# Kernel optimization log

Measured on AMD Instinct MI355X. Metric: run time of the kernel, lower is better.

The kernel has to match this reference:

```python
import jax, jax.numpy as jnp
import numpy as np

EPS = 1e-5
B, NA, T, D, H, L, DFF, E = 4, 64, 128, 128, 8, 3, 512, 65536
NN = T * NA  # nodes per graph = t*n after reshape(b, t*n, f)
DH = D // H


def _layer_norm(x, g, b):
    m = x.mean(-1, keepdims=True)
    v = ((x - m) ** 2).mean(-1, keepdims=True)
    return (x - m) * jax.lax.rsqrt(v + EPS) * g + b


def _pos_encoding(t, d):
    pos = jnp.arange(t, dtype=jnp.float32)[:, None]
    i = jnp.arange(0, d, 2, dtype=jnp.float32)
    ang = pos * jnp.exp(-jnp.log(10000.0) * i / d)
    pe = jnp.zeros((t, d), jnp.float32)
    return pe.at[:, 0::2].set(jnp.sin(ang)).at[:, 1::2].set(jnp.cos(ang))


def _forward(all_hist_feat, edge_weight, hist_w, hist_b,
             attn_wq, attn_bq, attn_wk, attn_bk, attn_wv, attn_bv, attn_wo, attn_bo,
             ln1_g, ln1_b, ff_w1, ff_b1, ff_w2, ff_b2, ln2_g, ln2_b,
             bn_g, bn_b, lin_graph_w, lin_graph_b, edge_index):
    b, n, t, _ = all_hist_feat.shape
    # history embedding: Linear(3, D)  -> [b, n, t, D]
    x = all_hist_feat @ hist_w + hist_b
    # sinusoidal positional encoding over the time axis
    out_e = x + _pos_encoding(t, D)
    scale = 1.0 / jnp.sqrt(jnp.asarray(DH, jnp.float32))
    for l in range(L):  # small fixed layer count
        q = out_e @ attn_wq[l] + attn_bq[l]
        k = out_e @ attn_wk[l] + attn_bk[l]
        v = out_e @ attn_wv[l] + attn_bv[l]
        qh = q.reshape(b, n, t, H, DH)
        kh = k.reshape(b, n, t, H, DH)
        vh = v.reshape(b, n, t, H, DH)
        scores = jnp.einsum('bnqhd,bnkhd->bnhqk', qh, kh) * scale
        attn = jax.nn.softmax(scores, axis=-1)
        o = jnp.einsum('bnhqk,bnkhd->bnqhd', attn, vh).reshape(b, n, t, D)
        o = o @ attn_wo[l] + attn_bo[l]
        h1 = _layer_norm(out_e + o, ln1_g[l], ln1_b[l])
        ff = jax.nn.relu(h1 @ ff_w1[l] + ff_b1[l]) @ ff_w2[l] + ff_b2[l]
        out_e = _layer_norm(h1 + ff, ln2_g[l], ln2_b[l])
    # graph stage: nodes are (time, agent) pairs, index = time*n + agent
    graph_w = out_e.transpose(0, 2, 1, 3).reshape(b, t * n, D)
    graph_x = x.transpose(0, 2, 1, 3).reshape(b, t * n, D)
    # GCNConv_Fixed_W (no self loops, no normalize): per-node score then
    # edge-weighted scatter-add from source to target (PyG convention)
    s = (graph_w * graph_x).sum(-1)  # [b, t*n]
    src, dst = edge_index[:, 0], edge_index[:, 1]

    def agg(s_b, src_b, dst_b, ew_b):
        return jax.ops.segment_sum(ew_b * s_b[src_b], dst_b, num_segments=NN)

    graph_out = jax.vmap(agg)(s, src, dst, edge_weight)  # [b, t*n]
    g = graph_out.reshape(b, t, n)
    # BatchNorm2d(1) on [b, 1, n, t]: single channel -> global batch stats
    m = g.mean()
    var = g.var()
    g = (g - m) * jax.lax.rsqrt(var + EPS) * bn_g[0] + bn_b[0]
    g4 = g.transpose(0, 2, 1)[..., None]  # [b, n, t, 1]
    return g4 @ lin_graph_w + lin_graph_b  # [b, n, t, D]


def setup_inputs() -> dict:
    keys = iter(jax.random.split(jax.random.key(0), 64))

    def nrm(shape, scale):
        return jax.random.normal(next(keys), shape, jnp.float32) * scale

    inp = {
        'all_hist_feat': nrm((B, NA, T, 3), 1.0),
        'edge_index': jax.random.randint(next(keys), (B, 2, E), 0, NN, jnp.int32),
        'edge_weight': jax.random.uniform(next(keys), (B, E), jnp.float32),
        'hist_w': nrm((3, D), 0.5), 'hist_b': nrm((D,), 0.02),
        'attn_wq': nrm((L, D, D), D ** -0.5), 'attn_bq': jnp.zeros((L, D)),
        'attn_wk': nrm((L, D, D), D ** -0.5), 'attn_bk': jnp.zeros((L, D)),
        'attn_wv': nrm((L, D, D), D ** -0.5), 'attn_bv': jnp.zeros((L, D)),
        'attn_wo': nrm((L, D, D), D ** -0.5), 'attn_bo': jnp.zeros((L, D)),
        'ln1_g': jnp.ones((L, D)), 'ln1_b': jnp.zeros((L, D)),
        'ff_w1': nrm((L, D, DFF), D ** -0.5), 'ff_b1': jnp.zeros((L, DFF)),
        'ff_w2': nrm((L, DFF, D), DFF ** -0.5), 'ff_b2': jnp.zeros((L, D)),
        'ln2_g': jnp.ones((L, D)), 'ln2_b': jnp.zeros((L, D)),
        'bn_g': jnp.ones((1,)), 'bn_b': jnp.zeros((1,)),
        'lin_graph_w': nrm((1, D), 1.0), 'lin_graph_b': jnp.zeros((D,)),
    }
    return inp


def reference(all_hist_feat, edge_index, edge_weight, hist_w, hist_b,
              attn_wq, attn_bq, attn_wk, attn_bk, attn_wv, attn_bv, attn_wo, attn_bo,
              ln1_g, ln1_b, ff_w1, ff_b1, ff_w2, ff_b2, ln2_g, ln2_b,
              bn_g, bn_b, lin_graph_w, lin_graph_b):
    return _forward(all_hist_feat, edge_weight, hist_w, hist_b,
                    attn_wq, attn_bq, attn_wk, attn_bk, attn_wv, attn_bv, attn_wo, attn_bo,
                    ln1_g, ln1_b, ff_w1, ff_b1, ff_w2, ff_b2, ln2_g, ln2_b,
                    bn_g, bn_b, lin_graph_w, lin_graph_b, edge_index)
```

## Files before the change

kernel.cpp:

```cpp
#include <hip/hip_runtime.h>
#include <hip/hip_bf16.h>
#include <math.h>

#define EPS_ 1e-5f
constexpr int B_ = 4, NA = 64, T_ = 128, D_ = 128, H_ = 8, L_ = 3, DFF = 512, E_ = 65536;
constexpr int DH = D_ / H_;
constexpr int NN = T_ * NA;
constexpr int NTOT = B_ * NA * T_;
constexpr int QLD = 384;
constexpr size_t NE_ = (size_t)NTOT * D_;

typedef __bf16 bf16x8 __attribute__((ext_vector_type(8)));
typedef float f32x4 __attribute__((ext_vector_type(4)));

__global__ __launch_bounds__(256) void embed_kernel(
    const float* __restrict__ hist, const float* __restrict__ w,
    const float* __restrict__ b, float* __restrict__ x, float* __restrict__ e) {
  int idx = blockIdx.x * 256 + threadIdx.x;
  if (idx >= NTOT * D_) return;
  int d = idx & (D_ - 1);
  int r = idx >> 7;
  int t = r & (T_ - 1);
  const float* hp = hist + (size_t)r * 3;
  float acc = b[d];
  acc += hp[0] * w[0 * D_ + d];
  acc += hp[1] * w[1 * D_ + d];
  acc += hp[2] * w[2 * D_ + d];
  x[idx] = acc;
  int p = d >> 1;
  float ang = (float)t * expf(-logf(10000.f) * (2.f * (float)p) / (float)D_);
  float pe = (d & 1) ? cosf(ang) : sinf(ang);
  e[idx] = acc + pe;
}

__global__ __launch_bounds__(256) void convert_weights(
    const float* __restrict__ wq, const float* __restrict__ wk,
    const float* __restrict__ wv, const float* __restrict__ wo,
    const float* __restrict__ w1, const float* __restrict__ w2,
    __bf16* __restrict__ hi, __bf16* __restrict__ lo) {
  const int LW = 196608;
  int idx = blockIdx.x * 256 + threadIdx.x;
  if (idx >= L_ * LW) return;
  int l = idx / LW;
  int rem = idx - l * LW;
  float src;
  int n, k, K, segoff;
  if (rem < 49152) {
    n = rem >> 7; k = rem & 127; K = 128; segoff = 0;
    int which = n >> 7, nl = n & 127;
    const float* W = (which == 0) ? wq : (which == 1) ? wk : wv;
    src = W[(size_t)l * 16384 + k * 128 + nl];
  } else if (rem < 65536) {
    int r2 = rem - 49152;
    n = r2 >> 7; k = r2 & 127; K = 128; segoff = 49152;
    src = wo[(size_t)l * 16384 + k * 128 + n];
  } else if (rem < 131072) {
    int r2 = rem - 65536;
    n = r2 >> 7; k = r2 & 127; K = 128; segoff = 65536;
    src = w1[(size_t)l * 65536 + k * 512 + n];
  } else {
    int r2 = rem - 131072;
    n = r2 >> 9; k = r2 & 511; K = 512; segoff = 131072;
    src = w2[(size_t)l * 65536 + k * 128 + n];
  }
  int nt = n >> 4, kt = k >> 5;
  int lane = ((k >> 3) & 3) * 16 + (n & 15);
  int j = k & 7;
  int dst = l * LW + segoff + ((nt * (K / 32) + kt) * 64 + lane) * 8 + j;
  __bf16 h = (__bf16)src;
  hi[dst] = h;
  lo[dst] = (__bf16)(src - (float)h);
}

__global__ __launch_bounds__(256) void bias_pack(
    const float* __restrict__ bq, const float* __restrict__ bk,
    const float* __restrict__ bv, float* __restrict__ pb) {
  int idx = blockIdx.x * 256 + threadIdx.x;
  if (idx >= L_ * QLD) return;
  int l = idx / QLD, n = idx - l * QLD;
  int which = n >> 7, nl = n & 127;
  const float* src = (which == 0) ? bq : (which == 1) ? bk : bv;
  pb[idx] = src[l * 128 + nl];
}

__device__ __forceinline__ void split8(const float* __restrict__ p,
                                       bf16x8& hi, bf16x8& lo) {
  float4 x0 = *(const float4*)p;
  float4 x1 = *(const float4*)(p + 4);
  float xv[8] = {x0.x, x0.y, x0.z, x0.w, x1.x, x1.y, x1.z, x1.w};
#pragma unroll
  for (int j = 0; j < 8; ++j) {
    __bf16 h = (__bf16)xv[j];
    hi[j] = h;
    lo[j] = (__bf16)(xv[j] - (float)h);
  }
}

__device__ __forceinline__ void cvt8(const float4& x0, const float4& x1,
                                     bf16x8& hi, bf16x8& lo) {
  float xv[8] = {x0.x, x0.y, x0.z, x0.w, x1.x, x1.y, x1.z, x1.w};
#pragma unroll
  for (int j = 0; j < 8; ++j) {
    __bf16 h = (__bf16)xv[j];
    hi[j] = h;
    lo[j] = (__bf16)(xv[j] - (float)h);
  }
}

#define GB_LOADA(buf, kt)                                                                  \
  {                                                                                        \
    _Pragma("unroll") for (int mf_ = 0; mf_ < 4; ++mf_) {                                  \
      const float* p_ = A + (size_t)(row0 + mf_ * 16 + m16) * lda + (kt) * 32 + quad * 8;  \
      ar[buf][mf_][0] = *(const float4*)p_;                                                \
      ar[buf][mf_][1] = *(const float4*)(p_ + 4);                                          \
    }                                                                                      \
  }
#define GB_LOADW(buf, kt)                                                                  \
  {                                                                                        \
    _Pragma("unroll") for (int nf_ = 0; nf_ < 4; ++nf_) {                                  \
      size_t off_ = ((size_t)(ctb + nf_) * (K / 32) + (kt)) * 512 + lane * 8;              \
      bh[buf][nf_] = *(const bf16x8*)(Whi + off_);                                         \
      bl[buf][nf_] = *(const bf16x8*)(Wlo + off_);                                         \
    }                                                                                      \
  }

template <int EPI, int K>
__global__ __launch_bounds__(256, 2) void gemm_big(
    const float* __restrict__ A, int lda,
    const __bf16* __restrict__ Whi, const __bf16* __restrict__ Wlo,
    const float* __restrict__ bias,
    float* __restrict__ C, int ldc) {
  const int wave = threadIdx.x >> 6;
  const int lane = threadIdx.x & 63;
  const int m16 = lane & 15;
  const int quad = lane >> 4;
  const int wrow = wave >> 1, wcol = wave & 1;
  const int row0 = blockIdx.y * 128 + wrow * 64;
  const int col0 = blockIdx.x * 128 + wcol * 64;
  const int ctb = col0 >> 4;

  f32x4 acc[4][4] = {};
  float4 ar[2][4][2];
  bf16x8 bh[2][4], bl[2][4];
  GB_LOADA(0, 0);
  GB_LOADW(0, 0);
#pragma unroll
  for (int kt = 0; kt < K / 32; ++kt) {
    const int cur = kt & 1, nxt = cur ^ 1;
    if (kt < K / 32 - 1) {
      GB_LOADA(nxt, kt + 1);
      GB_LOADW(nxt, kt + 1);
    }
    bf16x8 ahi[4], alo[4];
#pragma unroll
    for (int mf = 0; mf < 4; ++mf)
      cvt8(ar[cur][mf][0], ar[cur][mf][1], ahi[mf], alo[mf]);
#pragma unroll
    for (int mf = 0; mf < 4; ++mf)
#pragma unroll
      for (int nf = 0; nf < 4; ++nf) {
        acc[mf][nf] = __builtin_amdgcn_mfma_f32_16x16x32_bf16(ahi[mf], bh[cur][nf], acc[mf][nf], 0, 0, 0);
        acc[mf][nf] = __builtin_amdgcn_mfma_f32_16x16x32_bf16(ahi[mf], bl[cur][nf], acc[mf][nf], 0, 0, 0);
        acc[mf][nf] = __builtin_amdgcn_mfma_f32_16x16x32_bf16(alo[mf], bh[cur][nf], acc[mf][nf], 0, 0, 0);
      }
  }
#pragma unroll
  for (int mf = 0; mf < 4; ++mf)
#pragma unroll
    for (int nf = 0; nf < 4; ++nf) {
      int c = col0 + nf * 16 + m16;
      float bj = bias[c];
#pragma unroll
      for (int reg = 0; reg < 4; ++reg) {
        int r = row0 + mf * 16 + quad * 4 + reg;
        float v = acc[mf][nf][reg] + bj;
        if (EPI == 1) v = fmaxf(v, 0.f);
        C[(size_t)r * ldc + c] = v;
      }
    }
}
#undef GB_LOADA
#undef GB_LOADW

template <int K>
__global__ __launch_bounds__(256) void gemm_ln(
    const float* __restrict__ A, int lda,
    const __bf16* __restrict__ Whi, const __bf16* __restrict__ Wlo,
    const float* __restrict__ bias, const float* __restrict__ resid,
    const float* __restrict__ lng, const float* __restrict__ lnb,
    float* __restrict__ C) {
  const int wave = threadIdx.x >> 6;
  const int lane = threadIdx.x & 63;
  const int m16 = lane & 15;
  const int quad = lane >> 4;
  const int wrow = wave >> 1, wcol = wave & 1;
  const int row0 = blockIdx.y * 64 + wrow * 32;
  const int col0 = wcol * 64;
  const int ctb = wcol * 4;

  f32x4 acc[2][4] = {};
#pragma unroll
  for (int k0 = 0; k0 < K; k0 += 32) {
    bf16x8 ahi[2], alo[2];
#pragma unroll
    for (int mf = 0; mf < 2; ++mf)
      split8(A + (size_t)(row0 + mf * 16 + m16) * lda + k0 + quad * 8, ahi[mf], alo[mf]);
    bf16x8 bhi[4], blo[4];
#pragma unroll
    for (int nf = 0; nf < 4; ++nf) {
      size_t off = ((size_t)(ctb + nf) * (K / 32) + (k0 >> 5)) * 512 + lane * 8;
      bhi[nf] = *(const bf16x8*)(Whi + off);
      blo[nf] = *(const bf16x8*)(Wlo + off);
    }
#pragma unroll
    for (int mf = 0; mf < 2; ++mf)
#pragma unroll
      for (int nf = 0; nf < 4; ++nf) {
        acc[mf][nf] = __builtin_amdgcn_mfma_f32_16x16x32_bf16(ahi[mf], bhi[nf], acc[mf][nf], 0, 0, 0);
        acc[mf][nf] = __builtin_amdgcn_mfma_f32_16x16x32_bf16(ahi[mf], blo[nf], acc[mf][nf], 0, 0, 0);
        acc[mf][nf] = __builtin_amdgcn_mfma_f32_16x16x32_bf16(alo[mf], bhi[nf], acc[mf][nf], 0, 0, 0);
      }
  }
  __shared__ float rs[64][2], rq[64][2];
#pragma unroll
  for (int mf = 0; mf < 2; ++mf)
#pragma unroll
    for (int reg = 0; reg < 4; ++reg) {
      int lr = wrow * 32 + mf * 16 + quad * 4 + reg;
      int gr = blockIdx.y * 64 + lr;
      float s = 0.f, qq = 0.f;
#pragma unroll
      for (int nf = 0; nf < 4; ++nf) {
        int c = col0 + nf * 16 + m16;
        float v = acc[mf][nf][reg] + bias[c] + resid[(size_t)gr * 128 + c];
        acc[mf][nf][reg] = v;
        s += v;
        qq += v * v;
      }
#pragma unroll
      for (int off = 1; off < 16; off <<= 1) {
        s += __shfl_xor(s, off, 64);
        qq += __shfl_xor(qq, off, 64);
      }
      if (m16 == 0) { rs[lr][wcol] = s; rq[lr][wcol] = qq; }
    }
  __syncthreads();
#pragma unroll
  for (int mf = 0; mf < 2; ++mf)
#pragma unroll
    for (int reg = 0; reg < 4; ++reg) {
      int lr = wrow * 32 + mf * 16 + quad * 4 + reg;
      int gr = blockIdx.y * 64 + lr;
      float mean = (rs[lr][0] + rs[lr][1]) * (1.f / 128.f);
      float var = (rq[lr][0] + rq[lr][1]) * (1.f / 128.f) - mean * mean;
      float rstd = rsqrtf(var + EPS_);
#pragma unroll
      for (int nf = 0; nf < 4; ++nf) {
        int c = col0 + nf * 16 + m16;
        C[(size_t)gr * 128 + c] = (acc[mf][nf][reg] - mean) * rstd * lng[c] + lnb[c];
      }
    }
}

#define FF1_LOADA(buf, kt)                                                                  \
  {                                                                                         \
    _Pragma("unroll") for (int mf_ = 0; mf_ < 2; ++mf_) {                                   \
      const float* p_ = A + (size_t)(grow0 + mf_ * 16 + m16) * 128 + (kt) * 32 + quad * 8;  \
      ar[buf][mf_][0] = *(const float4*)p_;                                                 \
      ar[buf][mf_][1] = *(const float4*)(p_ + 4);                                           \
    }                                                                                       \
  }
#define FF1_LOADW(buf, kt)                                                                  \
  {                                                                                         \
    _Pragma("unroll") for (int nf_ = 0; nf_ < 8; ++nf_) {                                   \
      size_t off_ = ((size_t)(wave * 8 + nf_) * 4 + (kt)) * 512 + lane * 8;                 \
      bh[buf][nf_] = *(const bf16x8*)(W1hi + off_);                                         \
      bl[buf][nf_] = *(const bf16x8*)(W1lo + off_);                                         \
    }                                                                                       \
  }
#define FF2_LOADW(buf, kt)                                                                  \
  {                                                                                         \
    _Pragma("unroll") for (int nf_ = 0; nf_ < 2; ++nf_) {                                   \
      size_t off_ = ((size_t)(wave * 2 + nf_) * 16 + (kt)) * 512 + lane * 8;                \
      wh[buf][nf_] = *(const bf16x8*)(W2hi + off_);                                         \
      wl[buf][nf_] = *(const bf16x8*)(W2lo + off_);                                         \
    }                                                                                       \
  }

template <int SDOT>
__global__ __launch_bounds__(256, 2) void ff_fused(
    const float* __restrict__ A,
    const __bf16* __restrict__ W1hi, const __bf16* __restrict__ W1lo,
    const float* __restrict__ b1v,
    const __bf16* __restrict__ W2hi, const __bf16* __restrict__ W2lo,
    const float* __restrict__ b2v, const float* __restrict__ resid,
    const float* __restrict__ lng, const float* __restrict__ lnb,
    float* __restrict__ C,
    const float* __restrict__ bx, float* __restrict__ sdst) {
  extern __shared__ float Amid[];
  const int wave = threadIdx.x >> 6;
  const int lane = threadIdx.x & 63;
  const int m16 = lane & 15;
  const int quad = lane >> 4;
  const int grow0 = blockIdx.x * 32;

  {
    f32x4 acc[2][8] = {};
    float4 ar[2][2][2];
    bf16x8 bh[2][8], bl[2][8];
    FF1_LOADA(0, 0);
    FF1_LOADW(0, 0);
#pragma unroll
    for (int kt = 0; kt < 4; ++kt) {
      const int cur = kt & 1, nxt = cur ^ 1;
      if (kt < 3) {
        FF1_LOADA(nxt, kt + 1);
        FF1_LOADW(nxt, kt + 1);
      }
      bf16x8 ahi[2], alo[2];
#pragma unroll
      for (int mf = 0; mf < 2; ++mf)
        cvt8(ar[cur][mf][0], ar[cur][mf][1], ahi[mf], alo[mf]);
#pragma unroll
      for (int nf = 0; nf < 8; ++nf)
#pragma unroll
        for (int mf = 0; mf < 2; ++mf) {
          acc[mf][nf] = __builtin_amdgcn_mfma_f32_16x16x32_bf16(ahi[mf], bh[cur][nf], acc[mf][nf], 0, 0, 0);
          acc[mf][nf] = __builtin_amdgcn_mfma_f32_16x16x32_bf16(ahi[mf], bl[cur][nf], acc[mf][nf], 0, 0, 0);
          acc[mf][nf] = __builtin_amdgcn_mfma_f32_16x16x32_bf16(alo[mf], bh[cur][nf], acc[mf][nf], 0, 0, 0);
        }
    }
#pragma unroll
    for (int mf = 0; mf < 2; ++mf)
#pragma unroll
      for (int nf = 0; nf < 8; ++nf) {
        int c = wave * 128 + nf * 16 + m16;
        float bj = b1v[c];
#pragma unroll
        for (int reg = 0; reg < 4; ++reg) {
          int r = mf * 16 + quad * 4 + reg;
          Amid[r * 513 + c] = fmaxf(acc[mf][nf][reg] + bj, 0.f);
        }
      }
  }
  __syncthreads();

  f32x4 acc2[2][2] = {};
  {
    bf16x8 wh[2][2], wl[2][2];
    FF2_LOADW(0, 0);
#pragma unroll
    for (int kt = 0; kt < 16; ++kt) {
      const int cur = kt & 1;
      if (kt < 15) FF2_LOADW(cur ^ 1, kt + 1);
      bf16x8 ahi[2], alo[2];
#pragma unroll
      for (int mf = 0; mf < 2; ++mf)
        split8(&Amid[(mf * 16 + m16) * 513 + kt * 32 + quad * 8], ahi[mf], alo[mf]);
#pragma unroll
      for (int mf = 0; mf < 2; ++mf)
#pragma unroll
        for (int nf = 0; nf < 2; ++nf) {
          acc2[mf][nf] = __builtin_amdgcn_mfma_f32_16x16x32_bf16(ahi[mf], wh[cur][nf], acc2[mf][nf], 0, 0, 0);
          acc2[mf][nf] = __builtin_amdgcn_mfma_f32_16x16x32_bf16(ahi[mf], wl[cur][nf], acc2[mf][nf], 0, 0, 0);
          acc2[mf][nf] = __builtin_amdgcn_mfma_f32_16x16x32_bf16(alo[mf], wh[cur][nf], acc2[mf][nf], 0, 0, 0);
        }
    }
  }

  __shared__ float rs[32][4], rq[32][4], sd[32][4];
  const int col0 = wave * 32;
#pragma unroll
  for (int mf = 0; mf < 2; ++mf)
#pragma unroll
    for (int reg = 0; reg < 4; ++reg) {
      int lr = mf * 16 + quad * 4 + reg;
      int gr = grow0 + lr;
      float s = 0.f, qq = 0.f;
#pragma unroll
      for (int nf = 0; nf < 2; ++nf) {
        int c = col0 + nf * 16 + m16;
        float v = acc2[mf][nf][reg] + b2v[c] + resid[(size_t)gr * 128 + c];
        acc2[mf][nf][reg] = v;
        s += v;
        qq += v * v;
      }
#pragma unroll
      for (int off = 1; off < 16; off <<= 1) {
        s += __shfl_xor(s, off, 64);
        qq += __shfl_xor(qq, off, 64);
      }
      if (m16 == 0) { rs[lr][wave] = s; rq[lr][wave] = qq; }
    }
  __syncthreads();
#pragma unroll
  for (int mf = 0; mf < 2; ++mf)
#pragma unroll
    for (int reg = 0; reg < 4; ++reg) {
      int lr = mf * 16 + quad * 4 + reg;
      int gr = grow0 + lr;
      float mean = (rs[lr][0] + rs[lr][1] + rs[lr][2] + rs[lr][3]) * (1.f / 128.f);
      float var = (rq[lr][0] + rq[lr][1] + rq[lr][2] + rq[lr][3]) * (1.f / 128.f) - mean * mean;
      float rstd = rsqrtf(var + EPS_);
      float sdp = 0.f;
#pragma unroll
      for (int nf = 0; nf < 2; ++nf) {
        int c = col0 + nf * 16 + m16;
        float v = (acc2[mf][nf][reg] - mean) * rstd * lng[c] + lnb[c];
        C[(size_t)gr * 128 + c] = v;
        if (SDOT) sdp += v * bx[(size_t)gr * 128 + c];
      }
      if (SDOT) {
#pragma unroll
        for (int off = 1; off < 16; off <<= 1) sdp += __shfl_xor(sdp, off, 64);
        if (m16 == 0) sd[lr][wave] = sdp;
      }
    }
  if (SDOT) {
    __syncthreads();
    if (threadIdx.x < 32) {
      int lr = threadIdx.x;
      int gr = grow0 + lr;
      float sv = sd[lr][0] + sd[lr][1] + sd[lr][2] + sd[lr][3];
      int t = gr & (T_ - 1);
      int bn = gr >> 7;
      int n = bn & (NA - 1);
      int b = bn >> 6;
      sdst[(size_t)b * NN + t * NA + n] = sv;
    }
  }
}
#undef FF1_LOADA
#undef FF1_LOADW
#undef FF2_LOADW

__global__ __launch_bounds__(256) void attn_mfma(float* __restrict__ qkv) {
  const int h = blockIdx.x & (H_ - 1);
  const int bn = blockIdx.x >> 3;
  const int wave = threadIdx.x >> 6;
  const int lane = threadIdx.x & 63;
  const int m16 = lane & 15;
  const int quad = lane >> 4;
  const int row0 = wave * 32;
  const float* Qb = qkv + (size_t)bn * T_ * QLD + h * DH;
  const float* Kb = Qb + 128;
  const float* Vb = Qb + 256;
  float* Ob = (float*)Vb;

  __shared__ __bf16 Plds[4][32][136];
  __shared__ __bf16 KH[8][32][8], KL[8][32][8];
  __shared__ __bf16 VH[4][64][8], VL[4][64][8];

  for (int u = threadIdx.x; u < 1024; u += 256) {
    int isV = u >> 9;
    int r2 = u & 511;
    int t = r2 >> 2, c4 = r2 & 3;
    float4 v = *(const float4*)((isV ? Vb : Kb) + (size_t)t * QLD + c4 * 4);
    float xv[4] = {v.x, v.y, v.z, v.w};
#pragma unroll
    for (int i = 0; i < 4; ++i) {
      int dh = c4 * 4 + i;
      __bf16 hh = (__bf16)xv[i];
      __bf16 ll = (__bf16)(xv[i] - (float)hh);
      if (isV) {
        int kc = t >> 5, rem = t & 31;
        int vl = (rem >> 3) * 16 + dh;
        VH[kc][vl][rem & 7] = hh;
        VL[kc][vl][rem & 7] = ll;
      } else {
        int nf = t >> 4;
        int kl = (dh >> 3) * 16 + (t & 15);
        KH[nf][kl][dh & 7] = hh;
        KL[nf][kl][dh & 7] = ll;
      }
    }
  }

  bf16x8 qhi[2], qlo[2];
#pragma unroll
  for (int mf = 0; mf < 2; ++mf) {
    if (quad < 2) {
      split8(Qb + (size_t)(row0 + mf * 16 + m16) * QLD + quad * 8, qhi[mf], qlo[mf]);
    } else {
#pragma unroll
      for (int j = 0; j < 8; ++j) { qhi[mf][j] = (__bf16)0.f; qlo[mf][j] = (__bf16)0.f; }
    }
  }
  __syncthreads();

  f32x4 acc[2][8] = {};
#pragma unroll
  for (int nf = 0; nf < 8; ++nf) {
    bf16x8 khi, klo;
    if (quad < 2) {
      khi = *(const bf16x8*)&KH[nf][lane][0];
      klo = *(const bf16x8*)&KL[nf][lane][0];
    } else {
#pragma unroll
      for (int j = 0; j < 8; ++j) { khi[j] = (__bf16)0.f; klo[j] = (__bf16)0.f; }
    }
#pragma unroll
    for (int mf = 0; mf < 2; ++mf) {
      acc[mf][nf] = __builtin_amdgcn_mfma_f32_16x16x32_bf16(qhi[mf], khi, acc[mf][nf], 0, 0, 0);
      acc[mf][nf] = __builtin_amdgcn_mfma_f32_16x16x32_bf16(qhi[mf], klo, acc[mf][nf], 0, 0, 0);
      acc[mf][nf] = __builtin_amdgcn_mfma_f32_16x16x32_bf16(qlo[mf], khi, acc[mf][nf], 0, 0, 0);
    }
  }

  const float scale = 0.25f;
#pragma unroll
  for (int mf = 0; mf < 2; ++mf)
#pragma unroll
    for (int reg = 0; reg < 4; ++reg) {
      float mx = -1e30f;
#pragma unroll
      for (int nf = 0; nf < 8; ++nf) mx = fmaxf(mx, acc[mf][nf][reg]);
#pragma unroll
      for (int off = 1; off < 16; off <<= 1) mx = fmaxf(mx, __shfl_xor(mx, off, 64));
      float sum = 0.f;
#pragma unroll
      for (int nf = 0; nf < 8; ++nf) {
        float e = __expf((acc[mf][nf][reg] - mx) * scale);
        acc[mf][nf][reg] = e;
        sum += e;
      }
#pragma unroll
      for (int off = 1; off < 16; off <<= 1) sum += __shfl_xor(sum, off, 64);
      float inv = 1.f / sum;
#pragma unroll
      for (int nf = 0; nf < 8; ++nf) acc[mf][nf][reg] *= inv;
    }

#pragma unroll
  for (int mf = 0; mf < 2; ++mf)
#pragma unroll
    for (int nf = 0; nf < 8; ++nf)
#pragma unroll
      for (int reg = 0; reg < 4; ++reg)
        Plds[wave][mf * 16 + quad * 4 + reg][nf * 16 + m16] = (__bf16)acc[mf][nf][reg];

  f32x4 oacc[2] = {};
#pragma unroll
  for (int kc = 0; kc < 4; ++kc) {
    bf16x8 pa0 = *(const bf16x8*)&Plds[wave][m16][kc * 32 + quad * 8];
    bf16x8 pa1 = *(const bf16x8*)&Plds[wave][16 + m16][kc * 32 + quad * 8];
    bf16x8 vhi = *(const bf16x8*)&VH[kc][lane][0];
    bf16x8 vlo = *(const bf16x8*)&VL[kc][lane][0];
    oacc[0] = __builtin_amdgcn_mfma_f32_16x16x32_bf16(pa0, vhi, oacc[0], 0, 0, 0);
    oacc[0] = __builtin_amdgcn_mfma_f32_16x16x32_bf16(pa0, vlo, oacc[0], 0, 0, 0);
    oacc[1] = __builtin_amdgcn_mfma_f32_16x16x32_bf16(pa1, vhi, oacc[1], 0, 0, 0);
    oacc[1] = __builtin_amdgcn_mfma_f32_16x16x32_bf16(pa1, vlo, oacc[1], 0, 0, 0);
  }

#pragma unroll
  for (int mf = 0; mf < 2; ++mf)
#pragma unroll
    for (int reg = 0; reg < 4; ++reg) {
      int r = row0 + mf * 16 + quad * 4 + reg;
      Ob[(size_t)r * QLD + m16] = oacc[mf][reg];
    }
}

__global__ __launch_bounds__(256) void scatter_kernel(
    const float* __restrict__ s, const int* __restrict__ ei,
    const float* __restrict__ ew, float* __restrict__ g) {
  int idx = blockIdx.x * 256 + threadIdx.x;
  if (idx >= B_ * E_) return;
  int b = idx >> 16;
  int e = idx & (E_ - 1);
  int src = ei[(size_t)b * 2 * E_ + e];
  int dst = ei[(size_t)b * 2 * E_ + E_ + e];
  float w = ew[(size_t)b * E_ + e];
  atomicAdd(&g[(size_t)b * NN + dst], w * s[(size_t)b * NN + src]);
}

__global__ __launch_bounds__(256) void stats_partial(
    const float* __restrict__ g, float* __restrict__ st) {
  int i = blockIdx.x * 256 + threadIdx.x;
  float v = g[i];
  float sum = v, sq = v * v;
#pragma unroll
  for (int off = 32; off; off >>= 1) {
    sum += __shfl_down(sum, off, 64);
    sq += __shfl_down(sq, off, 64);
  }
  __shared__ float s1[4], s2[4];
  int w = threadIdx.x >> 6;
  if ((threadIdx.x & 63) == 0) { s1[w] = sum; s2[w] = sq; }
  __syncthreads();
  if (threadIdx.x == 0) {
    atomicAdd(&st[0], s1[0] + s1[1] + s1[2] + s1[3]);
    atomicAdd(&st[1], s2[0] + s2[1] + s2[2] + s2[3]);
  }
}

__global__ __launch_bounds__(256) void final_kernel(
    const float* __restrict__ g, const float* __restrict__ st,
    const float* __restrict__ bng, const float* __restrict__ bnb,
    const float* __restrict__ lw, const float* __restrict__ lb,
    float* __restrict__ out) {
  int idx = blockIdx.x * 256 + threadIdx.x;
  if (idx >= NTOT * D_) return;
  int d = idx & (D_ - 1);
  int r = idx >> 7;
  int t = r & (T_ - 1);
  int bn = r >> 7;
  int n = bn & (NA - 1);
  int b = bn >> 6;
  const float invn = 1.f / (float)(B_ * NN);
  float m = st[0] * invn;
  float var = st[1] * invn - m * m;
  float rs = rsqrtf(var + EPS_);
  float gv = g[(size_t)b * NN + t * NA + n];
  float val = (gv - m) * rs * bng[0] + bnb[0];
  out[idx] = val * lw[d] + lb[d];
}

extern "C" void kernel_launch(void* const* d_in, const int* in_sizes, int n_in,
                              void* d_out, int out_size, void* d_ws, size_t ws_size,
                              hipStream_t stream) {
  const float* hist = (const float*)d_in[0];
  const int* eidx = (const int*)d_in[1];
  const float* ew = (const float*)d_in[2];
  const float* hw = (const float*)d_in[3];
  const float* hb = (const float*)d_in[4];
  const float* wq = (const float*)d_in[5];
  const float* bq = (const float*)d_in[6];
  const float* wk = (const float*)d_in[7];
  const float* bk = (const float*)d_in[8];
  const float* wv = (const float*)d_in[9];
  const float* bv = (const float*)d_in[10];
  const float* wo = (const float*)d_in[11];
  const float* bo = (const float*)d_in[12];
  const float* ln1g = (const float*)d_in[13];
  const float* ln1b = (const float*)d_in[14];
  const float* w1 = (const float*)d_in[15];
  const float* b1 = (const float*)d_in[16];
  const float* w2 = (const float*)d_in[17];
  const float* b2 = (const float*)d_in[18];
  const float* ln2g = (const float*)d_in[19];
  const float* ln2b = (const float*)d_in[20];
  const float* bng = (const float*)d_in[21];
  const float* bnb = (const float*)d_in[22];
  const float* lgw = (const float*)d_in[23];
  const float* lgb = (const float*)d_in[24];
  float* out = (float*)d_out;

  float* ws = (float*)d_ws;
  const size_t NE = NE_;
  float* bx = ws + 0 * NE;
  float* be = ws + 1 * NE;
  float* h1 = ws + 2 * NE;
  float* qkv = ws + 3 * NE;
  float* bs_ = ws + 7 * NE;
  float* bg_ = bs_ + NTOT;
  float* bst = bg_ + NTOT;
  float* pbias = bst + 2;
  const int LW = 196608;
  __bf16* whiB = (__bf16*)(pbias + L_ * QLD);
  __bf16* wloB = whiB + (size_t)L_ * LW;

  const size_t ffshm = (size_t)32 * 513 * sizeof(float);
  static bool ff_attr_done = false;
  if (!ff_attr_done) {
    (void)hipFuncSetAttribute(reinterpret_cast<const void*>(&ff_fused<0>),
                              hipFuncAttributeMaxDynamicSharedMemorySize, (int)ffshm);
    (void)hipFuncSetAttribute(reinterpret_cast<const void*>(&ff_fused<1>),
                              hipFuncAttributeMaxDynamicSharedMemorySize, (int)ffshm);
    ff_attr_done = true;
  }

  convert_weights<<<(L_ * LW + 255) / 256, 256, 0, stream>>>(
      wq, wk, wv, wo, w1, w2, whiB, wloB);
  bias_pack<<<(L_ * QLD + 255) / 256, 256, 0, stream>>>(bq, bk, bv, pbias);
  embed_kernel<<<(NTOT * D_) / 256, 256, 0, stream>>>(hist, hw, hb, bx, be);

  for (int l = 0; l < L_; ++l) {
    const __bf16* hiL = whiB + (size_t)l * LW;
    const __bf16* loL = wloB + (size_t)l * LW;
    gemm_big<0, 128><<<dim3(3, NTOT / 128), 256, 0, stream>>>(
        be, 128, hiL, loL, pbias + l * QLD, qkv, QLD);
    attn_mfma<<<B_ * NA * H_, 256, 0, stream>>>(qkv);
    gemm_ln<128><<<dim3(1, NTOT / 64), 256, 0, stream>>>(
        qkv + 256, QLD, hiL + 49152, loL + 49152, bo + l * D_, be,
        ln1g + l * D_, ln1b + l * D_, h1);
    if (l < L_ - 1) {
      ff_fused<0><<<NTOT / 32, 256, ffshm, stream>>>(
          h1, hiL + 65536, loL + 65536, b1 + l * DFF,
          hiL + 131072, loL + 131072, b2 + l * D_, h1,
          ln2g + l * D_, ln2b + l * D_, be, nullptr, nullptr);
    } else {
      ff_fused<1><<<NTOT / 32, 256, ffshm, stream>>>(
          h1, hiL + 65536, loL + 65536, b1 + l * DFF,
          hiL + 131072, loL + 131072, b2 + l * D_, h1,
          ln2g + l * D_, ln2b + l * D_, be, bx, bs_);
    }
  }

  hipMemsetAsync(bg_, 0, ((size_t)B_ * NN + 2) * sizeof(float), stream);
  scatter_kernel<<<(B_ * E_) / 256, 256, 0, stream>>>(bs_, eidx, ew, bg_);
  stats_partial<<<(B_ * NN) / 256, 256, 0, stream>>>(bg_, bst);
  final_kernel<<<(NTOT * D_) / 256, 256, 0, stream>>>(bg_, bst, bng, bnb, lgw, lgb, out);
}
```

Before: 558.8 us.

## Stage FF weights via global_load_lds double buffers and preload split activations

The fused feed-forward kernel now streams W1/W2 hi/lo bf16 tiles straight into per-wave LDS double buffers with global_load_lds and explicit vmcnt waits, instead of holding them in registers. All four K-slices of the A input are split into hi/lo up front. Launch bounds drop to one block per SM, and dynamic shared memory grows by 64KB. The aim is lower register pressure and asynchronous weight prefetch overlapping the MFMA work, at the cost of occupancy and extra LDS reads.

New measurement: 610.5 us. 9.3% more time.

```diff
diff --git a/kernel.cpp b/kernel.cpp
--- a/kernel.cpp
+++ b/kernel.cpp
@@ -107,6 +107,12 @@
   }
 }
 
+__device__ __forceinline__ void gload16(const __bf16* g, __bf16* l) {
+  __builtin_amdgcn_global_load_lds(
+      (const __attribute__((address_space(1))) void*)g,
+      (__attribute__((address_space(3))) void*)l, 16, 0, 0);
+}
+
 #define GB_LOADA(buf, kt)                                                                  \
   {                                                                                        \
     _Pragma("unroll") for (int mf_ = 0; mf_ < 4; ++mf_) {                                  \
@@ -262,33 +268,28 @@
     }
 }
 
-#define FF1_LOADA(buf, kt)                                                                  \
-  {                                                                                         \
-    _Pragma("unroll") for (int mf_ = 0; mf_ < 2; ++mf_) {                                   \
-      const float* p_ = A + (size_t)(grow0 + mf_ * 16 + m16) * 128 + (kt) * 32 + quad * 8;  \
-      ar[buf][mf_][0] = *(const float4*)p_;                                                 \
-      ar[buf][mf_][1] = *(const float4*)(p_ + 4);                                           \
-    }                                                                                       \
-  }
-#define FF1_LOADW(buf, kt)                                                                  \
-  {                                                                                         \
-    _Pragma("unroll") for (int nf_ = 0; nf_ < 8; ++nf_) {                                   \
-      size_t off_ = ((size_t)(wave * 8 + nf_) * 4 + (kt)) * 512 + lane * 8;                 \
-      bh[buf][nf_] = *(const bf16x8*)(W1hi + off_);                                         \
-      bl[buf][nf_] = *(const bf16x8*)(W1lo + off_);                                         \
-    }                                                                                       \
-  }
-#define FF2_LOADW(buf, kt)                                                                  \
-  {                                                                                         \
-    _Pragma("unroll") for (int nf_ = 0; nf_ < 2; ++nf_) {                                   \
-      size_t off_ = ((size_t)(wave * 2 + nf_) * 16 + (kt)) * 512 + lane * 8;                \
-      wh[buf][nf_] = *(const bf16x8*)(W2hi + off_);                                         \
-      wl[buf][nf_] = *(const bf16x8*)(W2lo + off_);                                         \
-    }                                                                                       \
+#define FF1_STAGE(c, buf)                                                                    \
+  {                                                                                          \
+    const int kt_ = (c) >> 1, hf_ = (c) & 1;                                                 \
+    __bf16* dst_ = ws + (buf) * 4096;                                                        \
+    _Pragma("unroll") for (int j_ = 0; j_ < 4; ++j_) {                                       \
+      size_t off_ = ((size_t)(wave * 8 + hf_ * 4 + j_) * 4 + kt_) * 512 + lane * 8;          \
+      gload16(W1hi + off_, dst_ + j_ * 512);                                                 \
+      gload16(W1lo + off_, dst_ + (4 + j_) * 512);                                           \
+    }                                                                                        \
+  }
+#define FF2_STAGE(kt, buf)                                                                   \
+  {                                                                                          \
+    __bf16* dst_ = ws + (buf) * 4096;                                                        \
+    _Pragma("unroll") for (int nf_ = 0; nf_ < 2; ++nf_) {                                    \
+      size_t off_ = ((size_t)(wave * 2 + nf_) * 16 + (kt)) * 512 + lane * 8;                 \
+      gload16(W2hi + off_, dst_ + nf_ * 512);                                                \
+      gload16(W2lo + off_, dst_ + (2 + nf_) * 512);                                          \
+    }                                                                                        \
   }
 
 template <int SDOT>
-__global__ __launch_bounds__(256, 2) void ff_fused(
+__global__ __launch_bounds__(256, 1) void ff_fused(
     const float* __restrict__ A,
     const __bf16* __restrict__ W1hi, const __bf16* __restrict__ W1lo,
     const float* __restrict__ b1v,
@@ -303,32 +304,42 @@
   const int m16 = lane & 15;
   const int quad = lane >> 4;
   const int grow0 = blockIdx.x * 32;
+  __bf16* ws = (__bf16*)(Amid + 32 * 513) + wave * 8192;
+
+  bf16x8 ahi[4][2], alo[4][2];
+#pragma unroll
+  for (int kt = 0; kt < 4; ++kt)
+#pragma unroll
+    for (int mf = 0; mf < 2; ++mf)
+      split8(A + (size_t)(grow0 + mf * 16 + m16) * 128 + kt * 32 + quad * 8, ahi[kt][mf], alo[kt][mf]);
+  asm volatile("s_waitcnt vmcnt(0)" ::: "memory");
 
   {
     f32x4 acc[2][8] = {};
-    float4 ar[2][2][2];
-    bf16x8 bh[2][8], bl[2][8];
-    FF1_LOADA(0, 0);
-    FF1_LOADW(0, 0);
-#pragma unroll
-    for (int kt = 0; kt < 4; ++kt) {
-      const int cur = kt & 1, nxt = cur ^ 1;
-      if (kt < 3) {
-        FF1_LOADA(nxt, kt + 1);
-        FF1_LOADW(nxt, kt + 1);
-      }
-      bf16x8 ahi[2], alo[2];
-#pragma unroll
-      for (int mf = 0; mf < 2; ++mf)
-        cvt8(ar[cur][mf][0], ar[cur][mf][1], ahi[mf], alo[mf]);
-#pragma unroll
-      for (int nf = 0; nf < 8; ++nf)
+    FF1_STAGE(0, 0);
+#pragma unroll
+    for (int c = 0; c < 8; ++c) {
+      if (c < 7) {
+        FF1_STAGE(c + 1, (c + 1) & 1);
+        asm volatile("s_waitcnt vmcnt(8)" ::: "memory");
+      } else {
+        asm volatile("s_waitcnt vmcnt(0)" ::: "memory");
+      }
+      __builtin_amdgcn_sched_barrier(0);
+      const __bf16* src = ws + (c & 1) * 4096;
+      const int kt = c >> 1, hf = c & 1;
+#pragma unroll
+      for (int j = 0; j < 4; ++j) {
+        bf16x8 wh = *(const bf16x8*)(src + j * 512 + lane * 8);
+        bf16x8 wl = *(const bf16x8*)(src + (4 + j) * 512 + lane * 8);
+        const int nf = hf * 4 + j;
 #pragma unroll
         for (int mf = 0; mf < 2; ++mf) {
-          acc[mf][nf] = __builtin_amdgcn_mfma_f32_16x16x32_bf16(ahi[mf], bh[cur][nf], acc[mf][nf], 0, 0, 0);
-          acc[mf][nf] = __builtin_amdgcn_mfma_f32_16x16x32_bf16(ahi[mf], bl[cur][nf], acc[mf][nf], 0, 0, 0);
-          acc[mf][nf] = __builtin_amdgcn_mfma_f32_16x16x32_bf16(alo[mf], bh[cur][nf], acc[mf][nf], 0, 0, 0);
+          acc[mf][nf] = __builtin_amdgcn_mfma_f32_16x16x32_bf16(ahi[kt][mf], wh, acc[mf][nf], 0, 0, 0);
+          acc[mf][nf] = __builtin_amdgcn_mfma_f32_16x16x32_bf16(ahi[kt][mf], wl, acc[mf][nf], 0, 0, 0);
+          acc[mf][nf] = __builtin_amdgcn_mfma_f32_16x16x32_bf16(alo[kt][mf], wh, acc[mf][nf], 0, 0, 0);
         }
+      }
     }
 #pragma unroll
     for (int mf = 0; mf < 2; ++mf)
@@ -346,25 +357,31 @@
   __syncthreads();
 
   f32x4 acc2[2][2] = {};
-  {
-    bf16x8 wh[2][2], wl[2][2];
-    FF2_LOADW(0, 0);
-#pragma unroll
-    for (int kt = 0; kt < 16; ++kt) {
-      const int cur = kt & 1;
-      if (kt < 15) FF2_LOADW(cur ^ 1, kt + 1);
-      bf16x8 ahi[2], alo[2];
-#pragma unroll
-      for (int mf = 0; mf < 2; ++mf)
-        split8(&Amid[(mf * 16 + m16) * 513 + kt * 32 + quad * 8], ahi[mf], alo[mf]);
-#pragma unroll
-      for (int mf = 0; mf < 2; ++mf)
-#pragma unroll
-        for (int nf = 0; nf < 2; ++nf) {
-          acc2[mf][nf] = __builtin_amdgcn_mfma_f32_16x16x32_bf16(ahi[mf], wh[cur][nf], acc2[mf][nf], 0, 0, 0);
-          acc2[mf][nf] = __builtin_amdgcn_mfma_f32_16x16x32_bf16(ahi[mf], wl[cur][nf], acc2[mf][nf], 0, 0, 0);
-          acc2[mf][nf] = __builtin_amdgcn_mfma_f32_16x16x32_bf16(alo[mf], wh[cur][nf], acc2[mf][nf], 0, 0, 0);
-        }
+  FF2_STAGE(0, 0);
+#pragma unroll
+  for (int kt = 0; kt < 16; ++kt) {
+    if (kt < 15) {
+      FF2_STAGE(kt + 1, (kt + 1) & 1);
+      asm volatile("s_waitcnt vmcnt(4)" ::: "memory");
+    } else {
+      asm volatile("s_waitcnt vmcnt(0)" ::: "memory");
+    }
+    __builtin_amdgcn_sched_barrier(0);
+    const __bf16* src = ws + (kt & 1) * 4096;
+    bf16x8 phi[2], plo[2];
+#pragma unroll
+    for (int mf = 0; mf < 2; ++mf)
+      split8(&Amid[(mf * 16 + m16) * 513 + kt * 32 + quad * 8], phi[mf], plo[mf]);
+#pragma unroll
+    for (int nf = 0; nf < 2; ++nf) {
+      bf16x8 wh = *(const bf16x8*)(src + nf * 512 + lane * 8);
+      bf16x8 wl = *(const bf16x8*)(src + (2 + nf) * 512 + lane * 8);
+#pragma unroll
+      for (int mf = 0; mf < 2; ++mf) {
+        acc2[mf][nf] = __builtin_amdgcn_mfma_f32_16x16x32_bf16(phi[mf], wh, acc2[mf][nf], 0, 0, 0);
+        acc2[mf][nf] = __builtin_amdgcn_mfma_f32_16x16x32_bf16(phi[mf], wl, acc2[mf][nf], 0, 0, 0);
+        acc2[mf][nf] = __builtin_amdgcn_mfma_f32_16x16x32_bf16(plo[mf], wh, acc2[mf][nf], 0, 0, 0);
+      }
     }
   }
 
@@ -430,9 +447,8 @@
     }
   }
 }
-#undef FF1_LOADA
-#undef FF1_LOADW
-#undef FF2_LOADW
+#undef FF1_STAGE
+#undef FF2_STAGE
 
 __global__ __launch_bounds__(256) void attn_mfma(float* __restrict__ qkv) {
   const int h = blockIdx.x & (H_ - 1);
@@ -660,7 +676,7 @@
   __bf16* whiB = (__bf16*)(pbias + L_ * QLD);
   __bf16* wloB = whiB + (size_t)L_ * LW;
 
-  const size_t ffshm = (size_t)32 * 513 * sizeof(float);
+  const size_t ffshm = (size_t)32 * 513 * sizeof(float) + (size_t)4 * 2 * 4096 * sizeof(__bf16);
   static bool ff_attr_done = false;
   if (!ff_attr_done) {
     (void)hipFuncSetAttribute(reinterpret_cast<const void*>(&ff_fused<0>),
```
